# Performance work log

Hardware: AMD Instinct MI355X
Metric: run time of the kernel (lower is better)

The kernel has to match this reference:

```python
import jax, jax.numpy as jnp
import numpy as np
import math

B, S, DIM = 2, 2048, 1024
H, D = 16, 64  # num_head, head_dim; H*D == DIM

def setup_inputs() -> dict:
    key = jax.random.key(0)
    ks = jax.random.split(key, 10)
    s = 0.02
    return {
        "X": jax.random.normal(ks[0], (B, S, DIM), dtype=jnp.float32),
        "mask": jnp.ones((B, S), dtype=jnp.float32),
        "Wq": jax.random.normal(ks[1], (DIM, H * D), dtype=jnp.float32) * s,
        "bq": jnp.zeros((H * D,), dtype=jnp.float32),
        "Wk": jax.random.normal(ks[2], (DIM, H * D), dtype=jnp.float32) * s,
        "bk": jnp.zeros((H * D,), dtype=jnp.float32),
        "Wv": jax.random.normal(ks[3], (DIM, H * D), dtype=jnp.float32) * s,
        "bv": jnp.zeros((H * D,), dtype=jnp.float32),
        "Wo": jax.random.normal(ks[4], (H * D, DIM), dtype=jnp.float32) * s,
        "bo": jnp.zeros((DIM,), dtype=jnp.float32),
    }

def _split_heads(x):
    # [B, S, H*D] -> [B, H, S, D]
    b, s, _ = x.shape
    return x.reshape(b, s, H, D).transpose(0, 2, 1, 3)

def reference(X, mask, Wq, bq, Wk, bk, Wv, bv, Wo, bo):
    Q = _split_heads(X @ Wq + bq)
    K = _split_heads(X @ Wk + bk)
    V = _split_heads(X @ Wv + bv)
    # scaled dot-product attention with additive mask penalty
    dot = jnp.einsum('bhqd,bhkd->bhqk', Q, K) / math.sqrt(D)
    dot = dot - 1e6 * (1.0 - mask[:, None, None, :])
    attn = jax.nn.softmax(dot, axis=-1)
    ctx = jnp.einsum('bhqk,bhkd->bhqd', attn, V)
    # combine heads: [B, H, S, D] -> [B, S, H*D]
    ctx = ctx.transpose(0, 2, 1, 3).reshape(B, S, H * D)
    return ctx @ Wo + bo
```

## Files before the change

### kernel.cpp

```cpp
#include <hip/hip_runtime.h>
#include <cstdint>
#include <cstddef>

typedef __attribute__((ext_vector_type(8))) _Float16 f16x8;
typedef __attribute__((ext_vector_type(4))) _Float16 f16x4;
typedef __attribute__((ext_vector_type(4))) float f32x4;

#define MFMA_16x16x32(a, b, c) __builtin_amdgcn_mfma_f32_16x16x32_f16((a), (b), (c), 0, 0, 0)

static constexpr int kB = 2, kS = 2048, kDim = 1024, kH = 16, kD = 64;
static constexpr int kM = kB * kS;
static constexpr float kQScale = 0.125f * 1.44269504088896340736f;

__global__ void cvt_f32_to_f16(const float* __restrict__ in, _Float16* __restrict__ out, int n8) {
  int i = blockIdx.x * blockDim.x + threadIdx.x;
  if (i >= n8) return;
  const float4* p = (const float4*)in + (size_t)i * 2;
  float4 a = p[0], b = p[1];
  f16x8 h;
  h[0] = (_Float16)a.x; h[1] = (_Float16)a.y; h[2] = (_Float16)a.z; h[3] = (_Float16)a.w;
  h[4] = (_Float16)b.x; h[5] = (_Float16)b.y; h[6] = (_Float16)b.z; h[7] = (_Float16)b.w;
  ((f16x8*)out)[i] = h;
}

__global__ void transpose_cvt_w(const float* __restrict__ w0, const float* __restrict__ w1,
                                const float* __restrict__ w2, const float* __restrict__ w3,
                                _Float16* __restrict__ o0, _Float16* __restrict__ o1,
                                _Float16* __restrict__ o2, _Float16* __restrict__ o3) {
  const float* w; _Float16* o;
  switch (blockIdx.z) {
    case 0: w = w0; o = o0; break;
    case 1: w = w1; o = o1; break;
    case 2: w = w2; o = o2; break;
    default: w = w3; o = o3; break;
  }
  __shared__ alignas(16) _Float16 tile[64][72];
  const int kt = blockIdx.x * 64;
  const int nt = blockIdx.y * 64;
  const int tr = threadIdx.x >> 4;
  const int tc = threadIdx.x & 15;
#pragma unroll
  for (int rr = 0; rr < 4; ++rr) {
    int r = rr * 16 + tr;
    float4 v = *(const float4*)&w[(size_t)(kt + r) * kDim + nt + tc * 4];
    f16x4 hv;
    hv[0] = (_Float16)v.x; hv[1] = (_Float16)v.y; hv[2] = (_Float16)v.z; hv[3] = (_Float16)v.w;
    *(f16x4*)&tile[r][tc * 4] = hv;
  }
  __syncthreads();
#pragma unroll
  for (int rr = 0; rr < 4; ++rr) {
    int nl = rr * 16 + tr;
    f16x4 hv;
    hv[0] = tile[tc * 4 + 0][nl];
    hv[1] = tile[tc * 4 + 1][nl];
    hv[2] = tile[tc * 4 + 2][nl];
    hv[3] = tile[tc * 4 + 3][nl];
    *(f16x4*)&o[(size_t)(nt + nl) * kDim + kt + tc * 4] = hv;
  }
}

__global__ void mask_penalty(const float* __restrict__ mask, float* __restrict__ pen, int n) {
  int i = blockIdx.x * blockDim.x + threadIdx.x;
  if (i < n) pen[i] = -1.0e6f * (1.0f - mask[i]) * 1.44269504088896340736f;
}

__global__ __launch_bounds__(256, 2) void gemm_qkv(
    const _Float16* __restrict__ A,
    const _Float16* __restrict__ wt0, const _Float16* __restrict__ wt1, const _Float16* __restrict__ wt2,
    const float* __restrict__ bias0, const float* __restrict__ bias1, const float* __restrict__ bias2,
    _Float16* __restrict__ oq, _Float16* __restrict__ ok, _Float16* __restrict__ ov) {
  const _Float16* Bt; const float* bias; _Float16* out;
  switch (blockIdx.z) {
    case 0: Bt = wt0; bias = bias0; out = oq; break;
    case 1: Bt = wt1; bias = bias1; out = ok; break;
    default: Bt = wt2; bias = bias2; out = ov; break;
  }
  __shared__ alignas(16) _Float16 As[128 * 72];
  __shared__ alignas(16) _Float16 Bs[128 * 72];
  const int tid = threadIdx.x;
  const int lane = tid & 63;
  const int wave = tid >> 6;
  const int wm = wave & 1, wn = wave >> 1;
  const int l15 = lane & 15, quad = lane >> 4;
  const int m0 = blockIdx.x * 128, n0 = blockIdx.y * 128;

  f32x4 acc[4][4] = {};

  for (int k0 = 0; k0 < kDim; k0 += 64) {
    __syncthreads();
#pragma unroll
    for (int i = 0; i < 4; ++i) {
      int c = tid + 256 * i;
      int row = c >> 3, kc = (c & 7) * 8;
      *(f16x8*)&As[row * 72 + kc] = *(const f16x8*)&A[(size_t)(m0 + row) * kDim + k0 + kc];
      *(f16x8*)&Bs[row * 72 + kc] = *(const f16x8*)&Bt[(size_t)(n0 + row) * kDim + k0 + kc];
    }
    __syncthreads();
#pragma unroll
    for (int kk = 0; kk < 2; ++kk) {
      f16x8 af[4], bf[4];
#pragma unroll
      for (int t = 0; t < 4; ++t) af[t] = *(const f16x8*)&As[(wm * 64 + t * 16 + l15) * 72 + kk * 32 + quad * 8];
#pragma unroll
      for (int t = 0; t < 4; ++t) bf[t] = *(const f16x8*)&Bs[(wn * 64 + t * 16 + l15) * 72 + kk * 32 + quad * 8];
#pragma unroll
      for (int i = 0; i < 4; ++i)
#pragma unroll
        for (int j = 0; j < 4; ++j)
          acc[i][j] = MFMA_16x16x32(af[i], bf[j], acc[i][j]);
    }
  }

  const int mbase = m0 + wm * 64 + quad * 4;
  const int nbase = n0 + wn * 64 + l15;
  if (blockIdx.z == 2) {
#pragma unroll
    for (int j = 0; j < 4; ++j) {
      int n = nbase + j * 16;
      float bv = bias[n];
      int h = n >> 6, d = n & 63;
#pragma unroll
      for (int i = 0; i < 4; ++i) {
        int m = mbase + i * 16;
        int b = m >> 11, s = m & (kS - 1);
        f16x4 hv;
#pragma unroll
        for (int r = 0; r < 4; ++r) hv[r] = (_Float16)(acc[i][j][r] + bv);
        *(f16x4*)&out[((size_t)((b * kH + h) * kD + d)) * kS + s] = hv;
      }
    }
  } else {
    const float osc = (blockIdx.z == 0) ? kQScale : 1.0f;
#pragma unroll
    for (int j = 0; j < 4; ++j) {
      int n = nbase + j * 16;
      float bv = bias[n];
      int h = n >> 6, d = n & 63;
#pragma unroll
      for (int i = 0; i < 4; ++i) {
        int mrow = mbase + i * 16;
#pragma unroll
        for (int r = 0; r < 4; ++r) {
          int m = mrow + r;
          int b = m >> 11, s = m & (kS - 1);
          out[(size_t)(((b * kH + h) * kS) + s) * kD + d] = (_Float16)((acc[i][j][r] + bv) * osc);
        }
      }
    }
  }
}

__global__ __launch_bounds__(256, 2) void attn(
    const _Float16* __restrict__ Q, const _Float16* __restrict__ K,
    const _Float16* __restrict__ V, const float* __restrict__ pen2,
    _Float16* __restrict__ ctx) {
  const int bh = blockIdx.y;
  const int b = bh >> 4;
  const int q0 = blockIdx.x * 128;
  const int tid = threadIdx.x, lane = tid & 63, wave = tid >> 6;
  const int l15 = lane & 15, quad = lane >> 4;

  __shared__ alignas(16) _Float16 Ks[128 * 72];
  __shared__ alignas(16) _Float16 Vs[64 * 136];
  __shared__ alignas(16) _Float16 Pt[4][32 * 136];
  __shared__ alignas(16) float pens[128];

  const _Float16* Qh = Q + (size_t)bh * kS * kD;
  const _Float16* Kh = K + (size_t)bh * kS * kD;
  const _Float16* Vh = V + (size_t)bh * kS * kD;

  f16x8 qf[2][2];
#pragma unroll
  for (int t = 0; t < 2; ++t) {
    int qrow = q0 + wave * 32 + t * 16 + l15;
#pragma unroll
    for (int kk = 0; kk < 2; ++kk)
      qf[t][kk] = *(const f16x8*)&Qh[(size_t)qrow * kD + kk * 32 + quad * 8];
  }

  f32x4 o_acc[2][4] = {};
  float l_part[2] = {0.0f, 0.0f};

  for (int kb = 0; kb < kS; kb += 128) {
    __syncthreads();
#pragma unroll
    for (int i = 0; i < 4; ++i) {
      int c = tid + 256 * i;
      int row = c >> 3, dc = (c & 7) * 8;
      *(f16x8*)&Ks[row * 72 + dc] = *(const f16x8*)&Kh[(size_t)(kb + row) * kD + dc];
    }
#pragma unroll
    for (int i = 0; i < 4; ++i) {
      int c = tid + 256 * i;
      int row = c >> 4, sc8 = (c & 15) * 8;
      *(f16x8*)&Vs[row * 136 + sc8] = *(const f16x8*)&Vh[(size_t)row * kS + kb + sc8];
    }
    if (tid < 128) pens[tid] = pen2[b * kS + kb + tid];
    __syncthreads();

    f32x4 s[2][8] = {};
#pragma unroll
    for (int kk = 0; kk < 2; ++kk)
#pragma unroll
      for (int colt = 0; colt < 8; ++colt) {
        f16x8 kf = *(const f16x8*)&Ks[(colt * 16 + l15) * 72 + kk * 32 + quad * 8];
        s[0][colt] = MFMA_16x16x32(kf, qf[0][kk], s[0][colt]);
        s[1][colt] = MFMA_16x16x32(kf, qf[1][kk], s[1][colt]);
      }

#pragma unroll
    for (int t = 0; t < 2; ++t) {
#pragma unroll
      for (int colt = 0; colt < 8; ++colt) {
        f32x4 pn = *(const f32x4*)&pens[colt * 16 + quad * 4];
        f16x4 ph;
#pragma unroll
        for (int r = 0; r < 4; ++r) {
          float pv = __builtin_exp2f(s[t][colt][r] + pn[r]);
          l_part[t] += pv;
          ph[r] = (_Float16)pv;
        }
        *(f16x4*)&Pt[wave][(t * 16 + l15) * 136 + colt * 16 + quad * 4] = ph;
      }
    }

#pragma unroll
    for (int ks = 0; ks < 4; ++ks) {
      f16x8 pf0 = *(const f16x8*)&Pt[wave][(l15) * 136 + ks * 32 + quad * 8];
      f16x8 pf1 = *(const f16x8*)&Pt[wave][(16 + l15) * 136 + ks * 32 + quad * 8];
#pragma unroll
      for (int c = 0; c < 4; ++c) {
        f16x8 vf = *(const f16x8*)&Vs[(c * 16 + l15) * 136 + ks * 32 + quad * 8];
        o_acc[0][c] = MFMA_16x16x32(vf, pf0, o_acc[0][c]);
        o_acc[1][c] = MFMA_16x16x32(vf, pf1, o_acc[1][c]);
      }
    }
  }

  const int h = bh & 15;
#pragma unroll
  for (int t = 0; t < 2; ++t) {
    float lsum = l_part[t];
    lsum += __shfl_xor(lsum, 16, 64);
    lsum += __shfl_xor(lsum, 32, 64);
    float inv = 1.0f / lsum;
    int q = q0 + wave * 32 + t * 16 + l15;
#pragma unroll
    for (int c = 0; c < 4; ++c) {
      f16x4 oh;
#pragma unroll
      for (int r = 0; r < 4; ++r) oh[r] = (_Float16)(o_acc[t][c][r] * inv);
      *(f16x4*)&ctx[((size_t)(b * kS + q)) * kDim + h * kD + c * 16 + quad * 4] = oh;
    }
  }
}

__global__ __launch_bounds__(256, 2) void gemm_out(
    const _Float16* __restrict__ A, const _Float16* __restrict__ Bt,
    const float* __restrict__ bias, float* __restrict__ out) {
  __shared__ alignas(16) _Float16 As[128 * 72];
  __shared__ alignas(16) _Float16 Bs[128 * 72];
  const int tid = threadIdx.x;
  const int lane = tid & 63;
  const int wave = tid >> 6;
  const int wm = wave & 1, wn = wave >> 1;
  const int l15 = lane & 15, quad = lane >> 4;
  const int m0 = blockIdx.x * 128, n0 = blockIdx.y * 128;

  f32x4 acc[4][4] = {};

  for (int k0 = 0; k0 < kDim; k0 += 64) {
    __syncthreads();
#pragma unroll
    for (int i = 0; i < 4; ++i) {
      int c = tid + 256 * i;
      int row = c >> 3, kc = (c & 7) * 8;
      *(f16x8*)&As[row * 72 + kc] = *(const f16x8*)&A[(size_t)(m0 + row) * kDim + k0 + kc];
      *(f16x8*)&Bs[row * 72 + kc] = *(const f16x8*)&Bt[(size_t)(n0 + row) * kDim + k0 + kc];
    }
    __syncthreads();
#pragma unroll
    for (int kk = 0; kk < 2; ++kk) {
      f16x8 af[4], bf[4];
#pragma unroll
      for (int t = 0; t < 4; ++t) af[t] = *(const f16x8*)&As[(wm * 64 + t * 16 + l15) * 72 + kk * 32 + quad * 8];
#pragma unroll
      for (int t = 0; t < 4; ++t) bf[t] = *(const f16x8*)&Bs[(wn * 64 + t * 16 + l15) * 72 + kk * 32 + quad * 8];
#pragma unroll
      for (int i = 0; i < 4; ++i)
#pragma unroll
        for (int j = 0; j < 4; ++j)
          acc[i][j] = MFMA_16x16x32(af[i], bf[j], acc[i][j]);
    }
  }

  const int mbase = m0 + wm * 64 + quad * 4;
  const int nbase = n0 + wn * 64 + l15;
#pragma unroll
  for (int j = 0; j < 4; ++j) {
    int n = nbase + j * 16;
    float bv = bias[n];
#pragma unroll
    for (int i = 0; i < 4; ++i) {
      int mrow = mbase + i * 16;
#pragma unroll
      for (int r = 0; r < 4; ++r)
        out[(size_t)(mrow + r) * kDim + n] = acc[i][j][r] + bv;
    }
  }
}

extern "C" void kernel_launch(void* const* d_in, const int* in_sizes, int n_in,
                              void* d_out, int out_size, void* d_ws, size_t ws_size,
                              hipStream_t stream) {
  (void)in_sizes; (void)n_in; (void)out_size; (void)ws_size;
  const float* X    = (const float*)d_in[0];
  const float* mask = (const float*)d_in[1];
  const float* Wq   = (const float*)d_in[2];
  const float* bq   = (const float*)d_in[3];
  const float* Wk   = (const float*)d_in[4];
  const float* bk   = (const float*)d_in[5];
  const float* Wv   = (const float*)d_in[6];
  const float* bv   = (const float*)d_in[7];
  const float* Wo   = (const float*)d_in[8];
  const float* bo   = (const float*)d_in[9];
  float* out = (float*)d_out;

  char* ws = (char*)d_ws;
  _Float16* Xh   = (_Float16*)(ws);
  _Float16* Wqt  = (_Float16*)(ws + ((size_t)8  << 20));
  _Float16* Wkt  = (_Float16*)(ws + ((size_t)10 << 20));
  _Float16* Wvt  = (_Float16*)(ws + ((size_t)12 << 20));
  _Float16* Wot  = (_Float16*)(ws + ((size_t)14 << 20));
  _Float16* Qh   = (_Float16*)(ws + ((size_t)16 << 20));
  _Float16* Kh   = (_Float16*)(ws + ((size_t)24 << 20));
  _Float16* Vh   = (_Float16*)(ws + ((size_t)32 << 20));
  _Float16* Ch   = (_Float16*)(ws + ((size_t)40 << 20));
  float*    pen2 = (float*)   (ws + ((size_t)48 << 20));

  cvt_f32_to_f16<<<dim3(kM * kDim / 8 / 256), dim3(256), 0, stream>>>(X, Xh, kM * kDim / 8);
  transpose_cvt_w<<<dim3(16, 16, 4), dim3(256), 0, stream>>>(Wq, Wk, Wv, Wo, Wqt, Wkt, Wvt, Wot);
  mask_penalty<<<dim3(16), dim3(256), 0, stream>>>(mask, pen2, kB * kS);
  gemm_qkv<<<dim3(32, 8, 3), dim3(256), 0, stream>>>(Xh, Wqt, Wkt, Wvt, bq, bk, bv, Qh, Kh, Vh);
  attn<<<dim3(16, 32), dim3(256), 0, stream>>>(Qh, Kh, Vh, pen2, Ch);
  gemm_out<<<dim3(32, 8), dim3(256), 0, stream>>>(Ch, Wot, bo, out);
}
```

Measured before the change: 219.7 us.

## Load GEMM tiles directly into LDS with XOR-swizzled layout

Both projection GEMMs now fill their shared-memory tiles with global_load_lds (direct global-to-LDS DMA, 16 bytes per lane) instead of loading through registers. Because rows are written contiguously, the padded stride of 72 becomes 64 and bank conflicts are avoided with an XOR swizzle on the 8-element column chunk, applied on both the load and fragment-read sides. This removes VGPR staging and store instructions from the tile fill and shrinks LDS use. In exchange it relies on correct waitcnt handling for LDS DMA at the barrier, and the launch-bounds occupancy hint is dropped.

```diff
diff --git a/kernel.cpp b/kernel.cpp
--- a/kernel.cpp
+++ b/kernel.cpp
@@ -11,6 +11,12 @@
 static constexpr int kB = 2, kS = 2048, kDim = 1024, kH = 16, kD = 64;
 static constexpr int kM = kB * kS;
 static constexpr float kQScale = 0.125f * 1.44269504088896340736f;
+
+__device__ __forceinline__ void load_lds16(const _Float16* g, _Float16* l) {
+  __builtin_amdgcn_global_load_lds(
+      (const __attribute__((address_space(1))) void*)g,
+      (__attribute__((address_space(3))) void*)l, 16, 0, 0);
+}
 
 __global__ void cvt_f32_to_f16(const float* __restrict__ in, _Float16* __restrict__ out, int n8) {
   int i = blockIdx.x * blockDim.x + threadIdx.x;
@@ -65,7 +71,7 @@
   if (i < n) pen[i] = -1.0e6f * (1.0f - mask[i]) * 1.44269504088896340736f;
 }
 
-__global__ __launch_bounds__(256, 2) void gemm_qkv(
+__global__ __launch_bounds__(256) void gemm_qkv(
     const _Float16* __restrict__ A,
     const _Float16* __restrict__ wt0, const _Float16* __restrict__ wt1, const _Float16* __restrict__ wt2,
     const float* __restrict__ bias0, const float* __restrict__ bias1, const float* __restrict__ bias2,
@@ -76,8 +82,8 @@
     case 1: Bt = wt1; bias = bias1; out = ok; break;
     default: Bt = wt2; bias = bias2; out = ov; break;
   }
-  __shared__ alignas(16) _Float16 As[128 * 72];
-  __shared__ alignas(16) _Float16 Bs[128 * 72];
+  __shared__ alignas(16) _Float16 As[128 * 64];
+  __shared__ alignas(16) _Float16 Bs[128 * 64];
   const int tid = threadIdx.x;
   const int lane = tid & 63;
   const int wave = tid >> 6;
@@ -85,25 +91,30 @@
   const int l15 = lane & 15, quad = lane >> 4;
   const int m0 = blockIdx.x * 128, n0 = blockIdx.y * 128;
 
+  const int lrow = lane >> 3;
+  const int lc = (lane & 7) ^ lrow;
+  const int swz = l15 & 7;
+
   f32x4 acc[4][4] = {};
 
   for (int k0 = 0; k0 < kDim; k0 += 64) {
     __syncthreads();
 #pragma unroll
-    for (int i = 0; i < 4; ++i) {
-      int c = tid + 256 * i;
-      int row = c >> 3, kc = (c & 7) * 8;
-      *(f16x8*)&As[row * 72 + kc] = *(const f16x8*)&A[(size_t)(m0 + row) * kDim + k0 + kc];
-      *(f16x8*)&Bs[row * 72 + kc] = *(const f16x8*)&Bt[(size_t)(n0 + row) * kDim + k0 + kc];
+    for (int j = 0; j < 4; ++j) {
+      int row = wave * 32 + j * 8;
+      load_lds16(&A[(size_t)(m0 + row + lrow) * kDim + k0 + lc * 8], &As[row * 64]);
+      load_lds16(&Bt[(size_t)(n0 + row + lrow) * kDim + k0 + lc * 8], &Bs[row * 64]);
     }
     __syncthreads();
 #pragma unroll
     for (int kk = 0; kk < 2; ++kk) {
       f16x8 af[4], bf[4];
 #pragma unroll
-      for (int t = 0; t < 4; ++t) af[t] = *(const f16x8*)&As[(wm * 64 + t * 16 + l15) * 72 + kk * 32 + quad * 8];
-#pragma unroll
-      for (int t = 0; t < 4; ++t) bf[t] = *(const f16x8*)&Bs[(wn * 64 + t * 16 + l15) * 72 + kk * 32 + quad * 8];
+      for (int t = 0; t < 4; ++t)
+        af[t] = *(const f16x8*)&As[(wm * 64 + t * 16 + l15) * 64 + (((kk * 4 + quad) ^ swz) * 8)];
+#pragma unroll
+      for (int t = 0; t < 4; ++t)
+        bf[t] = *(const f16x8*)&Bs[(wn * 64 + t * 16 + l15) * 64 + (((kk * 4 + quad) ^ swz) * 8)];
 #pragma unroll
       for (int i = 0; i < 4; ++i)
 #pragma unroll
@@ -256,11 +267,11 @@
   }
 }
 
-__global__ __launch_bounds__(256, 2) void gemm_out(
+__global__ __launch_bounds__(256) void gemm_out(
     const _Float16* __restrict__ A, const _Float16* __restrict__ Bt,
     const float* __restrict__ bias, float* __restrict__ out) {
-  __shared__ alignas(16) _Float16 As[128 * 72];
-  __shared__ alignas(16) _Float16 Bs[128 * 72];
+  __shared__ alignas(16) _Float16 As[128 * 64];
+  __shared__ alignas(16) _Float16 Bs[128 * 64];
   const int tid = threadIdx.x;
   const int lane = tid & 63;
   const int wave = tid >> 6;
@@ -268,25 +279,30 @@
   const int l15 = lane & 15, quad = lane >> 4;
   const int m0 = blockIdx.x * 128, n0 = blockIdx.y * 128;
 
+  const int lrow = lane >> 3;
+  const int lc = (lane & 7) ^ lrow;
+  const int swz = l15 & 7;
+
   f32x4 acc[4][4] = {};
 
   for (int k0 = 0; k0 < kDim; k0 += 64) {
     __syncthreads();
 #pragma unroll
-    for (int i = 0; i < 4; ++i) {
-      int c = tid + 256 * i;
-      int row = c >> 3, kc = (c & 7) * 8;
-      *(f16x8*)&As[row * 72 + kc] = *(const f16x8*)&A[(size_t)(m0 + row) * kDim + k0 + kc];
-      *(f16x8*)&Bs[row * 72 + kc] = *(const f16x8*)&Bt[(size_t)(n0 + row) * kDim + k0 + kc];
+    for (int j = 0; j < 4; ++j) {
+      int row = wave * 32 + j * 8;
+      load_lds16(&A[(size_t)(m0 + row + lrow) * kDim + k0 + lc * 8], &As[row * 64]);
+      load_lds16(&Bt[(size_t)(n0 + row + lrow) * kDim + k0 + lc * 8], &Bs[row * 64]);
     }
     __syncthreads();
 #pragma unroll
     for (int kk = 0; kk < 2; ++kk) {
       f16x8 af[4], bf[4];
 #pragma unroll
-      for (int t = 0; t < 4; ++t) af[t] = *(const f16x8*)&As[(wm * 64 + t * 16 + l15) * 72 + kk * 32 + quad * 8];
-#pragma unroll
-      for (int t = 0; t < 4; ++t) bf[t] = *(const f16x8*)&Bs[(wn * 64 + t * 16 + l15) * 72 + kk * 32 + quad * 8];
+      for (int t = 0; t < 4; ++t)
+        af[t] = *(const f16x8*)&As[(wm * 64 + t * 16 + l15) * 64 + (((kk * 4 + quad) ^ swz) * 8)];
+#pragma unroll
+      for (int t = 0; t < 4; ++t)
+        bf[t] = *(const f16x8*)&Bs[(wn * 64 + t * 16 + l15) * 64 + (((kk * 4 + quad) ^ swz) * 8)];
 #pragma unroll
       for (int i = 0; i < 4; ++i)
 #pragma unroll
```

After: 226.8 us. +3.2%, slower.

## Load K/V fragments directly into registers and give each wave 64 query rows

Applied to the files above, without the earlier changes.

The attention kernel stops staging K, V and the penalty through shared memory behind block barriers. Each lane now loads its MFMA fragments of K, V and the penalty straight from global memory into registers, and each wave handles 64 query rows instead of 32. Blocks shrink to 128 threads with two waves, and only the per-wave P buffer stays in LDS. This removes both __syncthreads per tile and the LDS round trip, in exchange for many more registers, lower occupancy (launch bounds 128,1) and uncoalesced strided global loads that depend on cache hits.

```diff
diff --git a/kernel.cpp b/kernel.cpp
--- a/kernel.cpp
+++ b/kernel.cpp
@@ -151,106 +151,109 @@
   }
 }
 
-__global__ __launch_bounds__(256, 2) void attn(
+__global__ __launch_bounds__(128, 1) void attn(
     const _Float16* __restrict__ Q, const _Float16* __restrict__ K,
     const _Float16* __restrict__ V, const float* __restrict__ pen2,
     _Float16* __restrict__ ctx) {
   const int bh = blockIdx.y;
   const int b = bh >> 4;
-  const int q0 = blockIdx.x * 128;
+  const int h = bh & 15;
   const int tid = threadIdx.x, lane = tid & 63, wave = tid >> 6;
   const int l15 = lane & 15, quad = lane >> 4;
-
-  __shared__ alignas(16) _Float16 Ks[128 * 72];
-  __shared__ alignas(16) _Float16 Vs[64 * 136];
-  __shared__ alignas(16) _Float16 Pt[4][32 * 136];
-  __shared__ alignas(16) float pens[128];
+  const int q0w = blockIdx.x * 128 + wave * 64;
+
+  __shared__ alignas(16) _Float16 Pt[2][32 * 136];
 
   const _Float16* Qh = Q + (size_t)bh * kS * kD;
   const _Float16* Kh = K + (size_t)bh * kS * kD;
   const _Float16* Vh = V + (size_t)bh * kS * kD;
 
-  f16x8 qf[2][2];
-#pragma unroll
-  for (int t = 0; t < 2; ++t) {
-    int qrow = q0 + wave * 32 + t * 16 + l15;
+  f16x8 qf[4][2];
+#pragma unroll
+  for (int tt = 0; tt < 4; ++tt) {
+    int qrow = q0w + tt * 16 + l15;
 #pragma unroll
     for (int kk = 0; kk < 2; ++kk)
-      qf[t][kk] = *(const f16x8*)&Qh[(size_t)qrow * kD + kk * 32 + quad * 8];
-  }
-
-  f32x4 o_acc[2][4] = {};
-  float l_part[2] = {0.0f, 0.0f};
+      qf[tt][kk] = *(const f16x8*)&Qh[(size_t)qrow * kD + kk * 32 + quad * 8];
+  }
+
+  const _Float16* kbase = Kh + l15 * kD + quad * 8;
+  const _Float16* vbase0 = Vh + (size_t)l15 * kS + quad * 8;
+  const float* pbase = pen2 + b * kS + quad * 4;
+  _Float16* ptw = &Pt[wave][0];
+
+  f32x4 o_acc[4][4] = {};
+  float l_part[4] = {};
 
   for (int kb = 0; kb < kS; kb += 128) {
-    __syncthreads();
-#pragma unroll
-    for (int i = 0; i < 4; ++i) {
-      int c = tid + 256 * i;
-      int row = c >> 3, dc = (c & 7) * 8;
-      *(f16x8*)&Ks[row * 72 + dc] = *(const f16x8*)&Kh[(size_t)(kb + row) * kD + dc];
-    }
-#pragma unroll
-    for (int i = 0; i < 4; ++i) {
-      int c = tid + 256 * i;
-      int row = c >> 4, sc8 = (c & 15) * 8;
-      *(f16x8*)&Vs[row * 136 + sc8] = *(const f16x8*)&Vh[(size_t)row * kS + kb + sc8];
-    }
-    if (tid < 128) pens[tid] = pen2[b * kS + kb + tid];
-    __syncthreads();
-
-    f32x4 s[2][8] = {};
-#pragma unroll
-    for (int kk = 0; kk < 2; ++kk)
-#pragma unroll
-      for (int colt = 0; colt < 8; ++colt) {
-        f16x8 kf = *(const f16x8*)&Ks[(colt * 16 + l15) * 72 + kk * 32 + quad * 8];
-        s[0][colt] = MFMA_16x16x32(kf, qf[0][kk], s[0][colt]);
-        s[1][colt] = MFMA_16x16x32(kf, qf[1][kk], s[1][colt]);
+    f16x8 kf[2][8];
+#pragma unroll
+    for (int colt = 0; colt < 8; ++colt) {
+#pragma unroll
+      for (int kk = 0; kk < 2; ++kk)
+        kf[kk][colt] = *(const f16x8*)&kbase[(size_t)(kb + colt * 16) * kD + kk * 32];
+    }
+    f16x8 vf[4][4];
+#pragma unroll
+    for (int c = 0; c < 4; ++c)
+#pragma unroll
+      for (int ks = 0; ks < 4; ++ks)
+        vf[ks][c] = *(const f16x8*)&vbase0[(size_t)c * 16 * kS + kb + ks * 32];
+    f32x4 pn[8];
+#pragma unroll
+    for (int colt = 0; colt < 8; ++colt) pn[colt] = *(const f32x4*)&pbase[kb + colt * 16];
+
+#pragma unroll
+    for (int tp = 0; tp < 2; ++tp) {
+      f32x4 s[2][8] = {};
+#pragma unroll
+      for (int colt = 0; colt < 8; ++colt)
+#pragma unroll
+        for (int kk = 0; kk < 2; ++kk) {
+          s[0][colt] = MFMA_16x16x32(kf[kk][colt], qf[2 * tp][kk], s[0][colt]);
+          s[1][colt] = MFMA_16x16x32(kf[kk][colt], qf[2 * tp + 1][kk], s[1][colt]);
+        }
+#pragma unroll
+      for (int t01 = 0; t01 < 2; ++t01) {
+        float lp = 0.0f;
+#pragma unroll
+        for (int colt = 0; colt < 8; ++colt) {
+          f16x4 ph;
+#pragma unroll
+          for (int r = 0; r < 4; ++r) {
+            float pv = __builtin_exp2f(s[t01][colt][r] + pn[colt][r]);
+            lp += pv;
+            ph[r] = (_Float16)pv;
+          }
+          *(f16x4*)&ptw[(t01 * 16 + l15) * 136 + colt * 16 + quad * 4] = ph;
+        }
+        l_part[2 * tp + t01] += lp;
       }
-
-#pragma unroll
-    for (int t = 0; t < 2; ++t) {
-#pragma unroll
-      for (int colt = 0; colt < 8; ++colt) {
-        f32x4 pn = *(const f32x4*)&pens[colt * 16 + quad * 4];
-        f16x4 ph;
-#pragma unroll
-        for (int r = 0; r < 4; ++r) {
-          float pv = __builtin_exp2f(s[t][colt][r] + pn[r]);
-          l_part[t] += pv;
-          ph[r] = (_Float16)pv;
+#pragma unroll
+      for (int ks = 0; ks < 4; ++ks) {
+        f16x8 pf0 = *(const f16x8*)&ptw[l15 * 136 + ks * 32 + quad * 8];
+        f16x8 pf1 = *(const f16x8*)&ptw[(16 + l15) * 136 + ks * 32 + quad * 8];
+#pragma unroll
+        for (int c = 0; c < 4; ++c) {
+          o_acc[2 * tp][c] = MFMA_16x16x32(vf[ks][c], pf0, o_acc[2 * tp][c]);
+          o_acc[2 * tp + 1][c] = MFMA_16x16x32(vf[ks][c], pf1, o_acc[2 * tp + 1][c]);
         }
-        *(f16x4*)&Pt[wave][(t * 16 + l15) * 136 + colt * 16 + quad * 4] = ph;
       }
     }
-
-#pragma unroll
-    for (int ks = 0; ks < 4; ++ks) {
-      f16x8 pf0 = *(const f16x8*)&Pt[wave][(l15) * 136 + ks * 32 + quad * 8];
-      f16x8 pf1 = *(const f16x8*)&Pt[wave][(16 + l15) * 136 + ks * 32 + quad * 8];
-#pragma unroll
-      for (int c = 0; c < 4; ++c) {
-        f16x8 vf = *(const f16x8*)&Vs[(c * 16 + l15) * 136 + ks * 32 + quad * 8];
-        o_acc[0][c] = MFMA_16x16x32(vf, pf0, o_acc[0][c]);
-        o_acc[1][c] = MFMA_16x16x32(vf, pf1, o_acc[1][c]);
-      }
-    }
-  }
-
-  const int h = bh & 15;
-#pragma unroll
-  for (int t = 0; t < 2; ++t) {
-    float lsum = l_part[t];
+  }
+
+#pragma unroll
+  for (int tt = 0; tt < 4; ++tt) {
+    float lsum = l_part[tt];
     lsum += __shfl_xor(lsum, 16, 64);
     lsum += __shfl_xor(lsum, 32, 64);
     float inv = 1.0f / lsum;
-    int q = q0 + wave * 32 + t * 16 + l15;
+    int q = q0w + tt * 16 + l15;
 #pragma unroll
     for (int c = 0; c < 4; ++c) {
       f16x4 oh;
 #pragma unroll
-      for (int r = 0; r < 4; ++r) oh[r] = (_Float16)(o_acc[t][c][r] * inv);
+      for (int r = 0; r < 4; ++r) oh[r] = (_Float16)(o_acc[tt][c][r] * inv);
       *(f16x4*)&ctx[((size_t)(b * kS + q)) * kDim + h * kD + c * 16 + quad * 4] = oh;
     }
   }
@@ -343,6 +346,6 @@
   transpose_cvt_w<<<dim3(16, 16, 4), dim3(256), 0, stream>>>(Wq, Wk, Wv, Wo, Wqt, Wkt, Wvt, Wot);
   mask_penalty<<<dim3(16), dim3(256), 0, stream>>>(mask, pen2, kB * kS);
   gemm_qkv<<<dim3(32, 8, 3), dim3(256), 0, stream>>>(Xh, Wqt, Wkt, Wvt, bq, bk, bv, Qh, Kh, Vh);
-  attn<<<dim3(16, 32), dim3(256), 0, stream>>>(Qh, Kh, Vh, pen2, Ch);
+  attn<<<dim3(16, 32), dim3(128), 0, stream>>>(Qh, Kh, Vh, pen2, Ch);
   gemm_out<<<dim3(32, 8), dim3(256), 0, stream>>>(Ch, Wot, bo, out);
 }
```

Result: slower. 247.9 us (+12.8%).

## Load K/V/penalty fragments directly from global memory, drop shared staging and block syncs

Applied to the files above, without the earlier changes.

The attention kernel no longer stages K, V and the mask penalty in shared memory with two block-wide barriers per key tile. Instead each wave loads its MFMA operand fragments for K, V and the penalty straight from global memory into registers. Only the per-wave P transpose buffer stays in shared memory. This removes the barriers and the LDS traffic, but each of the four waves now fetches the same K/V data separately, relying on cache. It also raises register pressure, since 16 V fragments are held per tile.

```diff
diff --git a/kernel.cpp b/kernel.cpp
--- a/kernel.cpp
+++ b/kernel.cpp
@@ -157,14 +157,12 @@
     _Float16* __restrict__ ctx) {
   const int bh = blockIdx.y;
   const int b = bh >> 4;
-  const int q0 = blockIdx.x * 128;
+  const int h = bh & 15;
   const int tid = threadIdx.x, lane = tid & 63, wave = tid >> 6;
   const int l15 = lane & 15, quad = lane >> 4;
-
-  __shared__ alignas(16) _Float16 Ks[128 * 72];
-  __shared__ alignas(16) _Float16 Vs[64 * 136];
+  const int q0w = blockIdx.x * 128 + wave * 32;
+
   __shared__ alignas(16) _Float16 Pt[4][32 * 136];
-  __shared__ alignas(16) float pens[128];
 
   const _Float16* Qh = Q + (size_t)bh * kS * kD;
   const _Float16* Kh = K + (size_t)bh * kS * kD;
@@ -173,79 +171,76 @@
   f16x8 qf[2][2];
 #pragma unroll
   for (int t = 0; t < 2; ++t) {
-    int qrow = q0 + wave * 32 + t * 16 + l15;
+    int qrow = q0w + t * 16 + l15;
 #pragma unroll
     for (int kk = 0; kk < 2; ++kk)
       qf[t][kk] = *(const f16x8*)&Qh[(size_t)qrow * kD + kk * 32 + quad * 8];
   }
 
+  const _Float16* kbase = Kh + l15 * kD + quad * 8;
+  const _Float16* vbase = Vh + (size_t)l15 * kS + quad * 8;
+  const float* pbase = pen2 + b * kS + quad * 4;
+  _Float16* ptw = &Pt[wave][0];
+
   f32x4 o_acc[2][4] = {};
-  float l_part[2] = {0.0f, 0.0f};
+  float l_part[2] = {};
 
   for (int kb = 0; kb < kS; kb += 128) {
-    __syncthreads();
-#pragma unroll
-    for (int i = 0; i < 4; ++i) {
-      int c = tid + 256 * i;
-      int row = c >> 3, dc = (c & 7) * 8;
-      *(f16x8*)&Ks[row * 72 + dc] = *(const f16x8*)&Kh[(size_t)(kb + row) * kD + dc];
-    }
-#pragma unroll
-    for (int i = 0; i < 4; ++i) {
-      int c = tid + 256 * i;
-      int row = c >> 4, sc8 = (c & 15) * 8;
-      *(f16x8*)&Vs[row * 136 + sc8] = *(const f16x8*)&Vh[(size_t)row * kS + kb + sc8];
-    }
-    if (tid < 128) pens[tid] = pen2[b * kS + kb + tid];
-    __syncthreads();
+    f16x8 vf[4][4];
+#pragma unroll
+    for (int c = 0; c < 4; ++c)
+#pragma unroll
+      for (int ks = 0; ks < 4; ++ks)
+        vf[ks][c] = *(const f16x8*)&vbase[(size_t)c * 16 * kS + kb + ks * 32];
 
     f32x4 s[2][8] = {};
 #pragma unroll
-    for (int kk = 0; kk < 2; ++kk)
-#pragma unroll
-      for (int colt = 0; colt < 8; ++colt) {
-        f16x8 kf = *(const f16x8*)&Ks[(colt * 16 + l15) * 72 + kk * 32 + quad * 8];
-        s[0][colt] = MFMA_16x16x32(kf, qf[0][kk], s[0][colt]);
-        s[1][colt] = MFMA_16x16x32(kf, qf[1][kk], s[1][colt]);
-      }
-
-#pragma unroll
-    for (int t = 0; t < 2; ++t) {
-#pragma unroll
-      for (int colt = 0; colt < 8; ++colt) {
-        f32x4 pn = *(const f32x4*)&pens[colt * 16 + quad * 4];
+    for (int colt = 0; colt < 8; ++colt) {
+      f16x8 kf0 = *(const f16x8*)&kbase[(size_t)(kb + colt * 16) * kD];
+      f16x8 kf1 = *(const f16x8*)&kbase[(size_t)(kb + colt * 16) * kD + 32];
+      s[0][colt] = MFMA_16x16x32(kf0, qf[0][0], s[0][colt]);
+      s[1][colt] = MFMA_16x16x32(kf0, qf[1][0], s[1][colt]);
+      s[0][colt] = MFMA_16x16x32(kf1, qf[0][1], s[0][colt]);
+      s[1][colt] = MFMA_16x16x32(kf1, qf[1][1], s[1][colt]);
+    }
+
+#pragma unroll
+    for (int colt = 0; colt < 8; ++colt) {
+      f32x4 pn = *(const f32x4*)&pbase[kb + colt * 16];
+#pragma unroll
+      for (int t = 0; t < 2; ++t) {
         f16x4 ph;
+        float lp = 0.0f;
 #pragma unroll
         for (int r = 0; r < 4; ++r) {
           float pv = __builtin_exp2f(s[t][colt][r] + pn[r]);
-          l_part[t] += pv;
+          lp += pv;
           ph[r] = (_Float16)pv;
         }
-        *(f16x4*)&Pt[wave][(t * 16 + l15) * 136 + colt * 16 + quad * 4] = ph;
+        l_part[t] += lp;
+        *(f16x4*)&ptw[(t * 16 + l15) * 136 + colt * 16 + quad * 4] = ph;
       }
     }
 
 #pragma unroll
     for (int ks = 0; ks < 4; ++ks) {
-      f16x8 pf0 = *(const f16x8*)&Pt[wave][(l15) * 136 + ks * 32 + quad * 8];
-      f16x8 pf1 = *(const f16x8*)&Pt[wave][(16 + l15) * 136 + ks * 32 + quad * 8];
+      f16x8 pf0 = *(const f16x8*)&ptw[l15 * 136 + ks * 32 + quad * 8];
+      f16x8 pf1 = *(const f16x8*)&ptw[(16 + l15) * 136 + ks * 32 + quad * 8];
 #pragma unroll
       for (int c = 0; c < 4; ++c) {
-        f16x8 vf = *(const f16x8*)&Vs[(c * 16 + l15) * 136 + ks * 32 + quad * 8];
-        o_acc[0][c] = MFMA_16x16x32(vf, pf0, o_acc[0][c]);
-        o_acc[1][c] = MFMA_16x16x32(vf, pf1, o_acc[1][c]);
+        o_acc[0][c] = MFMA_16x16x32(vf[ks][c], pf0, o_acc[0][c]);
+        o_acc[1][c] = MFMA_16x16x32(vf[ks][c], pf1, o_acc[1][c]);
       }
     }
   }
 
-  const int h = bh & 15;
 #pragma unroll
   for (int t = 0; t < 2; ++t) {
     float lsum = l_part[t];
     lsum += __shfl_xor(lsum, 16, 64);
     lsum += __shfl_xor(lsum, 32, 64);
     float inv = 1.0f / lsum;
-    int q = q0 + wave * 32 + t * 16 + l15;
+    int q = q0w + t * 16 + l15;
 #pragma unroll
     for (int c = 0; c < 4; ++c) {
       f16x4 oh;
```

Result: slower. 299.3 us (+36.3%).
